# Kernel tuning notes

Hardware: AMD Instinct MI355X
Metric: run time of the kernel (lower is better)

## Reference

```python
import jax, jax.numpy as jnp
import numpy as np

HEADS = 6
DIM_HEAD = 64
SCALE = DIM_HEAD ** -0.5
BN_EPS = 1e-5


def _dw_pw(x, w_dw, gamma, beta, mean, var, w_pw, stride):
    """Depthwise 3x3 conv (groups=C) -> BatchNorm (inference) -> 1x1 pointwise conv."""
    C = x.shape[1]
    y = jax.lax.conv_general_dilated(
        x, w_dw, window_strides=(stride, stride), padding=((1, 1), (1, 1)),
        dimension_numbers=('NCHW', 'OIHW', 'NCHW'), feature_group_count=C)
    inv = gamma / jnp.sqrt(var + BN_EPS)
    y = y * inv[None, :, None, None] + (beta - mean * inv)[None, :, None, None]
    # 1x1 conv as einsum: w_pw is [O, C]
    return jnp.einsum('bchw,oc->bohw', y, w_pw)


def setup_inputs() -> dict:
    key = jax.random.key(0)
    ks = jax.random.split(key, 10)
    B, C, H, W = 32, 384, 32, 32
    inner = HEADS * DIM_HEAD  # 384
    ws = 0.05  # weight scale to keep attention logits sane
    return {
        'x': jax.random.normal(ks[0], (B, C, H, W), jnp.float32),
        'q_dw': jax.random.normal(ks[1], (C, 1, 3, 3), jnp.float32) * ws,
        'q_gamma': jnp.ones((C,), jnp.float32),
        'q_beta': jnp.zeros((C,), jnp.float32),
        'q_mean': jax.random.normal(ks[2], (C,), jnp.float32) * 0.1,
        'q_var': jax.random.uniform(ks[3], (C,), jnp.float32) + 0.5,
        'q_pw': jax.random.normal(ks[4], (inner, C), jnp.float32) * ws,
        'kv_dw': jax.random.normal(ks[5], (C, 1, 3, 3), jnp.float32) * ws,
        'kv_gamma': jnp.ones((C,), jnp.float32),
        'kv_beta': jnp.zeros((C,), jnp.float32),
        'kv_mean': jax.random.normal(ks[6], (C,), jnp.float32) * 0.1,
        'kv_var': jax.random.uniform(ks[7], (C,), jnp.float32) + 0.5,
        'kv_pw': jax.random.normal(ks[8], (2 * inner, C), jnp.float32) * ws,
        'out_w': jax.random.normal(ks[9], (C, inner), jnp.float32) * ws,
        'out_b': jnp.zeros((C,), jnp.float32),
    }


def reference(x, q_dw, q_gamma, q_beta, q_mean, q_var, q_pw,
              kv_dw, kv_gamma, kv_beta, kv_mean, kv_var, kv_pw,
              out_w, out_b):
    B, C, H, W = x.shape
    h, d = HEADS, DIM_HEAD
    # Q at full resolution, K/V spatially downsampled (stride 2)
    q = _dw_pw(x, q_dw, q_gamma, q_beta, q_mean, q_var, q_pw, stride=1)   # [B, h*d, H, W]
    kv = _dw_pw(x, kv_dw, kv_gamma, kv_beta, kv_mean, kv_var, kv_pw, stride=2)  # [B, 2*h*d, Hk, Wk]
    k, v = jnp.split(kv, 2, axis=1)
    Hk, Wk = k.shape[2], k.shape[3]
    # 'b (h d) x y -> b h (x y) d'
    q = q.reshape(B, h, d, H * W).transpose(0, 1, 3, 2)
    k = k.reshape(B, h, d, Hk * Wk).transpose(0, 1, 3, 2)
    v = v.reshape(B, h, d, Hk * Wk).transpose(0, 1, 3, 2)
    dots = jnp.einsum('bhid,bhjd->bhij', q, k) * SCALE  # [B, h, HW, HkWk]
    attn = jax.nn.softmax(dots, axis=-1)
    out = jnp.einsum('bhij,bhjd->bhid', attn, v)        # [B, h, HW, d]
    # 'b h (x y) d -> b (h d) x y'
    out = out.transpose(0, 1, 3, 2).reshape(B, h * d, H, W)
    # final 1x1 conv projection (dropout is identity, p=0)
    return jnp.einsum('bchw,oc->bohw', out, out_w) + out_b[None, :, None, None]
```

## Files before the change

### kernel.cpp

```cpp
#include <hip/hip_runtime.h>
#include <hip/hip_bf16.h>

#define CIN 384
#define PQ 1024
#define PKV 256
#define HEADS 6
#define DH 64
#define INNER 384
#define ATTN_SCALE 0.125f

typedef __hip_bfloat16 bf16;
typedef unsigned short ushort;
typedef __bf16 bf16x8 __attribute__((ext_vector_type(8)));
typedef float floatx4 __attribute__((ext_vector_type(4)));

__device__ __forceinline__ float b2f(bf16 v) { return __bfloat162float(v); }
__device__ __forceinline__ bf16 f2b(float v) { return __float2bfloat16(v); }
__device__ __forceinline__ ushort f2bu(float v) { bf16 h = __float2bfloat16(v); return *(ushort*)&h; }
__device__ __forceinline__ float ldf(const void* p, size_t i, int isbf) {
    return isbf ? __bfloat162float(((const bf16*)p)[i]) : ((const float*)p)[i];
}
__device__ __forceinline__ void dma16(const bf16* g, bf16* l) {
    __builtin_amdgcn_global_load_lds(
        (const __attribute__((address_space(1))) unsigned int*)g,
        (__attribute__((address_space(3))) unsigned int*)l, 16, 0, 0);
}
__device__ __forceinline__ int probe_isbf(const void* x) {
    const unsigned* u = (const unsigned*)x;
    int cnt = 0;
    for (int i = 0; i < 64; i++) {
        unsigned e = (u[i] >> 7) & 0xFFu;
        cnt += (e >= 100u && e <= 140u) ? 1 : 0;
    }
    return cnt >= 48 ? 1 : 0;
}
__device__ __forceinline__ unsigned cvtpk(float lo, float hi) {
    unsigned r;
    asm("v_cvt_pk_bf16_f32 %0, %1, %2" : "=v"(r) : "v"(lo), "v"(hi));
    return r;
}
__device__ __forceinline__ void halfswap(unsigned a, unsigned b, unsigned& lo, unsigned& hi) {
#if __has_builtin(__builtin_amdgcn_permlane32_swap)
    auto r = __builtin_amdgcn_permlane32_swap(a, b, false, false);
    lo = r[0]; hi = r[1];
#else
    unsigned ax = (unsigned)__shfl_xor((int)a, 32, 64);
    unsigned bx = (unsigned)__shfl_xor((int)b, 32, 64);
    bool lower = (threadIdx.x & 32) == 0;
    lo = lower ? a : bx;
    hi = lower ? ax : b;
#endif
}

template <int STRIDE, int HO, int WO>
__global__ __launch_bounds__(256) void dw_bn_kernel(
        const void* __restrict__ x, const void* __restrict__ wdw,
        const void* __restrict__ gamma, const void* __restrict__ beta,
        const void* __restrict__ mean, const void* __restrict__ var,
        bf16* __restrict__ yt,
        const void* __restrict__ w0, const void* __restrict__ w1,
        const void* __restrict__ w2, bf16* __restrict__ wdst) {
    constexpr int IN_ROWS = (8 - 1) * STRIDE + 3;
    constexpr int RL = 37;
    constexpr int PT = 8 * WO;
    constexpr unsigned XSZ = 32u * IN_ROWS * RL * 4;
    constexpr unsigned OSZ = (unsigned)PT * 40 * 2;
    __shared__ __align__(16) char smem[XSZ > OSZ ? XSZ : OSZ];
    float (*xin)[IN_ROWS][RL] = (float (*)[IN_ROWS][RL])smem;
    ushort (*outt)[40] = (ushort (*)[40])smem;

    int isbf = probe_isbf(x);
    int rg = blockIdx.x;
    int c0 = blockIdx.y * 32;
    int b  = blockIdx.z;
    int tid = threadIdx.x;

    if (c0 >= CIN) {
        const int n0 = INNER * CIN, n1 = 2 * INNER * CIN, n2 = INNER * CIN;
        const int total = n0 + n1 + n2;
        for (int i = (b * 4 + rg) * 256 + tid; i < total; i += 32768) {
            float v;
            if (i < n0) v = ldf(w0, i, isbf);
            else if (i < n0 + n1) v = ldf(w1, i - n0, isbf);
            else v = ldf(w2, i - n0 - n1, isbf);
            wdst[i] = f2b(v);
        }
        return;
    }

    int ri0 = rg * 8 * STRIDE - 1;

    for (int e = tid; e < 32 * IN_ROWS; e += 256) {
        int i = e % IN_ROWS, cc = e / IN_ROWS;
        xin[cc][i][0] = 0.f;
        xin[cc][i][33] = 0.f;
    }

    const int NCHUNK = 32 * IN_ROWS * 4;
    for (int ch = tid; ch < NCHUNK; ch += 256) {
        int wc = ch & 3;
        int t  = ch >> 2;
        int i  = t % IN_ROWS;
        int cc = t / IN_ROWS;
        int row = ri0 + i;
        float f[8];
        if (row >= 0 && row < 32) {
            size_t goff = ((size_t)(b * CIN + c0 + cc) * 32 + row) * 32 + wc * 8;
            if (isbf) {
                uint4 v = *(const uint4*)((const bf16*)x + goff);
                const ushort* u = (const ushort*)&v;
#pragma unroll
                for (int j = 0; j < 8; j++) f[j] = __uint_as_float((unsigned)u[j] << 16);
            } else {
                float4 v0 = *(const float4*)((const float*)x + goff);
                float4 v1 = *(const float4*)((const float*)x + goff + 4);
                f[0] = v0.x; f[1] = v0.y; f[2] = v0.z; f[3] = v0.w;
                f[4] = v1.x; f[5] = v1.y; f[6] = v1.z; f[7] = v1.w;
            }
        } else {
#pragma unroll
            for (int j = 0; j < 8; j++) f[j] = 0.f;
        }
        float* dst = &xin[cc][i][1 + wc * 8];
#pragma unroll
        for (int j = 0; j < 8; j++) dst[j] = f[j];
    }

    int cc = tid & 31;
    int g  = tid >> 5;
    int c  = c0 + cc;
    float w9[9];
#pragma unroll
    for (int k = 0; k < 9; k++) w9[k] = ldf(wdw, c * 9 + k, isbf);
    float inv  = ldf(gamma, c, isbf) * rsqrtf(ldf(var, c, isbf) + 1e-5f);
    float bias = ldf(beta, c, isbf) - ldf(mean, c, isbf) * inv;
    __syncthreads();

    const float* xr0 = xin[cc][g * STRIDE + 0];
    const float* xr1 = xin[cc][g * STRIDE + 1];
    const float* xr2 = xin[cc][g * STRIDE + 2];
    float o[WO];
    if (STRIDE == 1) {
        float a0 = xr0[0], a1 = xr0[1];
        float b0 = xr1[0], b1 = xr1[1];
        float q0 = xr2[0], q1 = xr2[1];
#pragma unroll
        for (int wo = 0; wo < WO; wo++) {
            float a2 = xr0[wo + 2], b2 = xr1[wo + 2], q2 = xr2[wo + 2];
            float acc = w9[0] * a0 + w9[1] * a1 + w9[2] * a2
                      + w9[3] * b0 + w9[4] * b1 + w9[5] * b2
                      + w9[6] * q0 + w9[7] * q1 + w9[8] * q2;
            o[wo] = acc * inv + bias;
            a0 = a1; a1 = a2; b0 = b1; b1 = b2; q0 = q1; q1 = q2;
        }
    } else {
        float a0 = xr0[0], b0 = xr1[0], q0 = xr2[0];
#pragma unroll
        for (int wo = 0; wo < WO; wo++) {
            float a1 = xr0[2 * wo + 1], a2 = xr0[2 * wo + 2];
            float b1 = xr1[2 * wo + 1], b2 = xr1[2 * wo + 2];
            float q1 = xr2[2 * wo + 1], q2 = xr2[2 * wo + 2];
            float acc = w9[0] * a0 + w9[1] * a1 + w9[2] * a2
                      + w9[3] * b0 + w9[4] * b1 + w9[5] * b2
                      + w9[6] * q0 + w9[7] * q1 + w9[8] * q2;
            o[wo] = acc * inv + bias;
            a0 = a2; b0 = b2; q0 = q2;
        }
    }
    __syncthreads();

#pragma unroll
    for (int wo = 0; wo < WO; wo++) outt[g * WO + wo][cc] = f2bu(o[wo]);
    __syncthreads();

    const size_t pbase = (size_t)b * (HO * WO) + (size_t)rg * 8 * WO;
    for (int chk = tid; chk < PT * 4; chk += 256) {
        int k = chk & 3, p = chk >> 2;
        uint4 v = *(const uint4*)&outt[p][k * 8];
        *(uint4*)(yt + (pbase + p) * CIN + c0 + k * 8) = v;
    }
}

__global__ __launch_bounds__(256, 3) void mfma_pw_qkv(
        const bf16* __restrict__ qpw, const bf16* __restrict__ yqt,
        bf16* __restrict__ qalt,
        const bf16* __restrict__ kvpw, const bf16* __restrict__ ykvt,
        bf16* __restrict__ kalt, bf16* __restrict__ valt) {
    __shared__ __align__(16) bf16 As[2][4096];
    __shared__ __align__(16) bf16 Bs[2][4096];
    int tid = threadIdx.x;
    int wave = tid >> 6, lane = tid & 63;
    int l15 = lane & 15, quad = lane >> 4;
    int wm = wave & 1, wn = wave >> 1;

    int bid = blockIdx.x;
    int P, b, p0, o0;
    const bf16 *asrc0, *bsrc0;
    bf16* outq;
    if (bid < 768) {
        int m = bid;
        int p0t = m & 7; m >>= 3;
        int o0t = m % 3; b = m / 3;
        P = 1024; p0 = p0t * 128; o0 = o0t * 128;
        asrc0 = yqt; bsrc0 = qpw; outq = qalt;
    } else {
        int m = bid - 768;
        int p0t = m & 1; m >>= 1;
        int o0t = m % 6; b = m / 6;
        P = 256; p0 = p0t * 128; o0 = o0t * 128;
        asrc0 = ykvt; bsrc0 = kvpw; outq = kalt;
    }

    const bf16* asrc = asrc0 + ((size_t)b * P + p0) * CIN;
    const bf16* bsrc = bsrc0 + (size_t)o0 * CIN;

    int srow = (lane >> 2);
    int sc   = lane & 3;
    auto stage = [&](int step, int buf) {
#pragma unroll
        for (int it = 0; it < 2; it++) {
            int row = wave * 32 + it * 16 + srow;
            int g = sc ^ (row & 3);
            size_t goff = (size_t)row * CIN + step * 32 + g * 8;
            dma16(asrc + goff, &As[buf][(wave * 2 + it) * 512]);
            dma16(bsrc + goff, &Bs[buf][(wave * 2 + it) * 512]);
        }
    };

    floatx4 acc[4][4];
#pragma unroll
    for (int pt = 0; pt < 4; pt++)
#pragma unroll
        for (int ot = 0; ot < 4; ot++) acc[pt][ot] = (floatx4){0.f, 0.f, 0.f, 0.f};

    stage(0, 0);
    __syncthreads();
    for (int s = 0; s < CIN / 32; s++) {
        int buf = s & 1;
        if (s < CIN / 32 - 1) stage(s + 1, buf ^ 1);
        bf16x8 af[4], bw[4];
        int slot = (quad ^ (l15 & 3)) * 8;
#pragma unroll
        for (int pt = 0; pt < 4; pt++)
            af[pt] = *(const bf16x8*)&As[buf][(wm * 64 + pt * 16 + l15) * 32 + slot];
#pragma unroll
        for (int ot = 0; ot < 4; ot++)
            bw[ot] = *(const bf16x8*)&Bs[buf][(wn * 64 + ot * 16 + l15) * 32 + slot];
#pragma unroll
        for (int pt = 0; pt < 4; pt++)
#pragma unroll
            for (int ot = 0; ot < 4; ot++)
                acc[pt][ot] = __builtin_amdgcn_mfma_f32_16x16x32_bf16(af[pt], bw[ot], acc[pt][ot], 0, 0, 0);
        __syncthreads();
    }

    int pw0 = p0 + wm * 64, ow0 = o0 + wn * 64;
#pragma unroll
    for (int ot = 0; ot < 4; ot++) {
        int o = ow0 + ot * 16 + l15;
        if (o < INNER) {
            int h = o >> 6, d = o & 63;
            bf16* base = outq + ((size_t)(b * HEADS + h) * P) * 64 + d;
#pragma unroll
            for (int pt = 0; pt < 4; pt++)
#pragma unroll
                for (int r = 0; r < 4; r++)
                    base[(size_t)(pw0 + pt * 16 + quad * 4 + r) * 64] = f2b(acc[pt][ot][r]);
        } else {
            int ch = o - INNER;
            bf16* base = valt + ((size_t)b * INNER + ch) * PKV;
#pragma unroll
            for (int pt = 0; pt < 4; pt++)
#pragma unroll
                for (int r = 0; r < 4; r++)
                    base[pw0 + pt * 16 + quad * 4 + r] = f2b(acc[pt][ot][r]);
        }
    }
}

__global__ __launch_bounds__(256, 3) void mfma_pw_out(
        const bf16* __restrict__ wt, const bf16* __restrict__ yt,
        const void* __restrict__ bias, void* __restrict__ out0,
        const void* __restrict__ xprobe) {
    __shared__ __align__(16) bf16 As[2][4096];
    __shared__ __align__(16) bf16 Bs[2][4096];
    const int P = PQ, O = CIN;
    int tid = threadIdx.x;
    int wave = tid >> 6, lane = tid & 63;
    int l15 = lane & 15, quad = lane >> 4;
    int wm = wave & 1, wn = wave >> 1;
    int b = blockIdx.z;
    int p0 = blockIdx.x * 128;
    int o0 = blockIdx.y * 128;

    const bf16* asrc = yt + ((size_t)b * P + p0) * CIN;
    const bf16* bsrc = wt + (size_t)o0 * CIN;

    int srow = (lane >> 2);
    int sc   = lane & 3;
    auto stage = [&](int step, int buf) {
#pragma unroll
        for (int it = 0; it < 2; it++) {
            int row = wave * 32 + it * 16 + srow;
            int g = sc ^ (row & 3);
            size_t goff = (size_t)row * CIN + step * 32 + g * 8;
            dma16(asrc + goff, &As[buf][(wave * 2 + it) * 512]);
            dma16(bsrc + goff, &Bs[buf][(wave * 2 + it) * 512]);
        }
    };

    floatx4 acc[4][4];
#pragma unroll
    for (int pt = 0; pt < 4; pt++)
#pragma unroll
        for (int ot = 0; ot < 4; ot++) acc[pt][ot] = (floatx4){0.f, 0.f, 0.f, 0.f};

    stage(0, 0);
    __syncthreads();
    for (int s = 0; s < CIN / 32; s++) {
        int buf = s & 1;
        if (s < CIN / 32 - 1) stage(s + 1, buf ^ 1);
        bf16x8 af[4], bw[4];
        int slot = (quad ^ (l15 & 3)) * 8;
#pragma unroll
        for (int pt = 0; pt < 4; pt++)
            af[pt] = *(const bf16x8*)&As[buf][(wm * 64 + pt * 16 + l15) * 32 + slot];
#pragma unroll
        for (int ot = 0; ot < 4; ot++)
            bw[ot] = *(const bf16x8*)&Bs[buf][(wn * 64 + ot * 16 + l15) * 32 + slot];
#pragma unroll
        for (int pt = 0; pt < 4; pt++)
#pragma unroll
            for (int ot = 0; ot < 4; ot++)
                acc[pt][ot] = __builtin_amdgcn_mfma_f32_16x16x32_bf16(af[pt], bw[ot], acc[pt][ot], 0, 0, 0);
        __syncthreads();
    }

    int pw0 = p0 + wm * 64, ow0 = o0 + wn * 64;
    int isbf = probe_isbf(xprobe);
#pragma unroll
    for (int ot = 0; ot < 4; ot++) {
        int o = ow0 + ot * 16 + l15;
        float bv = ldf(bias, o, isbf);
#pragma unroll
        for (int pt = 0; pt < 4; pt++) {
            int p = pw0 + pt * 16 + quad * 4;
            size_t idx = ((size_t)b * O + o) * P + p;
            if (!isbf) {
                float4 v4 = {acc[pt][ot][0] + bv, acc[pt][ot][1] + bv,
                             acc[pt][ot][2] + bv, acc[pt][ot][3] + bv};
                *(float4*)((float*)out0 + idx) = v4;
            } else {
                ushort4 u4 = {f2bu(acc[pt][ot][0] + bv), f2bu(acc[pt][ot][1] + bv),
                              f2bu(acc[pt][ot][2] + bv), f2bu(acc[pt][ot][3] + bv)};
                *(ushort4*)((bf16*)out0 + idx) = u4;
            }
        }
    }
}

#define QKT(S, Q0, Q1)                                                              \
    do {                                                                            \
        floatx4 z_ = (floatx4){0.f, 0.f, 0.f, 0.f};                                 \
        _Pragma("unroll")                                                           \
        for (int jt_ = 0; jt_ < 16; jt_++) {                                        \
            int j_ = jt_ * 16 + l15;                                                \
            bf16x8 k0_ = *(const bf16x8*)&Kl[j_ * 64 + (quad ^ (j_ & 7)) * 8];      \
            bf16x8 k1_ = *(const bf16x8*)&Kl[j_ * 64 + ((4 + quad) ^ (j_ & 7)) * 8];\
            floatx4 t_ = __builtin_amdgcn_mfma_f32_16x16x32_bf16(k0_, Q0, z_, 0, 0, 0); \
            S[jt_] = __builtin_amdgcn_mfma_f32_16x16x32_bf16(k1_, Q1, t_, 0, 0, 0); \
        }                                                                           \
    } while (0)

#define SOFTMAX(S, PINV)                                                            \
    do {                                                                            \
        float m0_ = S[0][0], m1_ = S[0][1], m2_ = S[0][2], m3_ = S[0][3];           \
        _Pragma("unroll")                                                           \
        for (int jt_ = 1; jt_ < 16; jt_++) {                                        \
            m0_ = fmaxf(m0_, S[jt_][0]); m1_ = fmaxf(m1_, S[jt_][1]);               \
            m2_ = fmaxf(m2_, S[jt_][2]); m3_ = fmaxf(m3_, S[jt_][3]);               \
        }                                                                           \
        float mx_ = fmaxf(fmaxf(m0_, m1_), fmaxf(m2_, m3_));                        \
        mx_ = fmaxf(mx_, __shfl_xor(mx_, 16, 64));                                  \
        mx_ = fmaxf(mx_, __shfl_xor(mx_, 32, 64));                                  \
        float mc_ = mx_ * C;                                                        \
        float a0_ = 0.f, a1_ = 0.f, a2_ = 0.f, a3_ = 0.f;                           \
        _Pragma("unroll")                                                           \
        for (int jt_ = 0; jt_ < 16; jt_++) {                                        \
            float e0_ = exp2f(S[jt_][0] * C - mc_);                                 \
            float e1_ = exp2f(S[jt_][1] * C - mc_);                                 \
            float e2_ = exp2f(S[jt_][2] * C - mc_);                                 \
            float e3_ = exp2f(S[jt_][3] * C - mc_);                                 \
            S[jt_][0] = e0_; S[jt_][1] = e1_; S[jt_][2] = e2_; S[jt_][3] = e3_;     \
            a0_ += e0_; a1_ += e1_; a2_ += e2_; a3_ += e3_;                         \
        }                                                                           \
        float sm_ = (a0_ + a1_) + (a2_ + a3_);                                      \
        sm_ += __shfl_xor(sm_, 16, 64);                                             \
        sm_ += __shfl_xor(sm_, 32, 64);                                             \
        PINV = 1.f / sm_;                                                           \
    } while (0)

#define PV_STORE(S, PINV, T)                                                        \
    do {                                                                            \
        floatx4 oacc_[4];                                                           \
        _Pragma("unroll")                                                           \
        for (int nt_ = 0; nt_ < 4; nt_++) oacc_[nt_] = (floatx4){0.f, 0.f, 0.f, 0.f}; \
        _Pragma("unroll")                                                           \
        for (int kk_ = 0; kk_ < 8; kk_++) {                                         \
            floatx4 se_ = S[2 * kk_], so_ = S[2 * kk_ + 1];                         \
            unsigned E0_ = cvtpk(se_[0] * PINV, se_[1] * PINV);                     \
            unsigned E1_ = cvtpk(se_[2] * PINV, se_[3] * PINV);                     \
            unsigned D0_ = cvtpk(so_[0] * PINV, so_[1] * PINV);                     \
            unsigned D1_ = cvtpk(so_[2] * PINV, so_[3] * PINV);                     \
            unsigned lo0_, hi0_, lo1_, hi1_;                                        \
            halfswap(E0_, D0_, lo0_, hi0_);                                         \
            halfswap(E1_, D1_, lo1_, hi1_);                                         \
            unsigned sel0_ = (quad & 1) ? hi0_ : lo0_;                              \
            unsigned sel1_ = (quad & 1) ? hi1_ : lo1_;                              \
            unsigned x0_ = (unsigned)__shfl_xor((int)sel0_, 16, 64);                \
            unsigned x1_ = (unsigned)__shfl_xor((int)sel1_, 16, 64);                \
            union { unsigned u[4]; bf16x8 v; } pf_;                                 \
            pf_.u[0] = (quad & 1) ? x0_ : sel0_;                                    \
            pf_.u[1] = (quad & 1) ? x1_ : sel1_;                                    \
            pf_.u[2] = (quad & 1) ? sel0_ : x0_;                                    \
            pf_.u[3] = (quad & 1) ? sel1_ : x1_;                                    \
            _Pragma("unroll")                                                       \
            for (int nt_ = 0; nt_ < 4; nt_++) {                                     \
                int d_ = nt_ * 16 + l15;                                            \
                bf16x8 bv_ = *(const bf16x8*)&Vl[d_ * 256 + ((kk_ * 4 + quad) ^ (d_ & 15)) * 8]; \
                oacc_[nt_] = __builtin_amdgcn_mfma_f32_16x16x32_bf16(pf_.v, bv_, oacc_[nt_], 0, 0, 0); \
            }                                                                       \
        }                                                                           \
        _Pragma("unroll")                                                           \
        for (int nt_ = 0; nt_ < 4; nt_++)                                           \
            _Pragma("unroll")                                                       \
            for (int r_ = 0; r_ < 4; r_++)                                          \
                Ot[wave][quad * 4 + r_][nt_ * 16 + l15] = f2bu(oacc_[nt_][r_]);     \
        int row_ = lane >> 2, d0_ = (lane & 3) * 16;                                \
        uint4 ld0_ = *(const uint4*)&Ot[wave][row_][d0_];                           \
        uint4 ld1_ = *(const uint4*)&Ot[wave][row_][d0_ + 8];                       \
        bf16* dst_ = ao + ((size_t)b * PQ + p0 + (T) * 64 + row_) * INNER + h * DH + d0_; \
        *(uint4*)dst_ = ld0_;                                                       \
        *(uint4*)(dst_ + 8) = ld1_;                                                 \
    } while (0)

__global__ __launch_bounds__(256, 2) void attn_kernel(
        const bf16* __restrict__ qalt, const bf16* __restrict__ kalt,
        const bf16* __restrict__ valt, bf16* __restrict__ ao) {
    __shared__ __align__(16) bf16 Kl[16384];
    __shared__ __align__(16) bf16 Vl[16384];
    __shared__ __align__(16) ushort Ot[4][16][80];
    int tid = threadIdx.x;
    int wave = tid >> 6, lane = tid & 63;
    int l15 = lane & 15, quad = lane >> 4;
    int blk = blockIdx.x;
    int swz = (blk & 7) * 96 + (blk >> 3);
    int seg = swz & 3;
    int bh  = swz >> 2;
    int b = bh / HEADS, h = bh % HEADS;

    const bf16* qbase = qalt + (size_t)(b * HEADS + h) * PQ * DH;
    const bf16* kbase = kalt + (size_t)(b * HEADS + h) * PKV * DH;
    const bf16* vbase = valt + ((size_t)b * INNER + h * DH) * PKV;

    {
        int j = lane >> 3, cs = lane & 7;
#pragma unroll
        for (int it = 0; it < 8; it++) {
            int jr = (wave * 8 + it) * 8 + j;
            int g = cs ^ (jr & 7);
            dma16(kbase + (size_t)jr * 64 + g * 8, &Kl[(wave * 8 + it) * 512]);
        }
        int d = lane >> 5, cs2 = lane & 31;
#pragma unroll
        for (int it = 0; it < 8; it++) {
            int dr = (wave * 8 + it) * 2 + d;
            int g = cs2 ^ (dr & 15);
            dma16(vbase + (size_t)dr * 256 + g * 8, &Vl[(wave * 8 + it) * 512]);
        }
    }

    int p0 = seg * 256 + wave * 16;
    const bf16* qrow = qbase + (size_t)(p0 + l15) * DH + quad * 8;
    bf16x8 qA0 = *(const bf16x8*)qrow;
    bf16x8 qA1 = *(const bf16x8*)(qrow + 32);
    bf16x8 qB0 = *(const bf16x8*)(qrow + 64 * DH);
    bf16x8 qB1 = *(const bf16x8*)(qrow + 64 * DH + 32);
    __syncthreads();

    const float C = ATTN_SCALE * 1.44269504f;
    floatx4 sA[16], sB[16];
    float pinv;

    QKT(sA, qA0, qA1);
    qA0 = *(const bf16x8*)(qrow + 128 * DH);
    qA1 = *(const bf16x8*)(qrow + 128 * DH + 32);

    SOFTMAX(sA, pinv);
    QKT(sB, qB0, qB1);
    PV_STORE(sA, pinv, 0);
    qB0 = *(const bf16x8*)(qrow + 192 * DH);
    qB1 = *(const bf16x8*)(qrow + 192 * DH + 32);

    SOFTMAX(sB, pinv);
    QKT(sA, qA0, qA1);
    PV_STORE(sB, pinv, 1);

    SOFTMAX(sA, pinv);
    QKT(sB, qB0, qB1);
    PV_STORE(sA, pinv, 2);

    SOFTMAX(sB, pinv);
    PV_STORE(sB, pinv, 3);
}

extern "C" void kernel_launch(void* const* d_in, const int* in_sizes, int n_in,
                              void* d_out, int out_size, void* d_ws, size_t ws_size,
                              hipStream_t stream) {
    const void* x        = d_in[0];
    const void* q_dw     = d_in[1];
    const void* q_gamma  = d_in[2];
    const void* q_beta   = d_in[3];
    const void* q_mean   = d_in[4];
    const void* q_var    = d_in[5];
    const void* q_pw     = d_in[6];
    const void* kv_dw    = d_in[7];
    const void* kv_gamma = d_in[8];
    const void* kv_beta  = d_in[9];
    const void* kv_mean  = d_in[10];
    const void* kv_var   = d_in[11];
    const void* kv_pw    = d_in[12];
    const void* out_w    = d_in[13];
    const void* out_b    = d_in[14];

    bf16* pool = (bf16*)((char*)d_ws + 256);
    bf16* yqt  = pool;
    bf16* ykvt = yqt  + (size_t)32 * 1024 * 384;
    bf16* qalt = ykvt + (size_t)32 * 256 * 384;
    bf16* kalt = qalt + (size_t)32 * 6 * 1024 * 64;
    bf16* valt = kalt + (size_t)32 * 6 * 256 * 64;
    bf16* wbf  = valt + (size_t)32 * 384 * 256;
    bf16* qpw_bf = wbf;
    bf16* kvpw_bf = wbf + (size_t)INNER * CIN;
    bf16* outw_bf = kvpw_bf + (size_t)2 * INNER * CIN;
    bf16* aob  = yqt;

    dw_bn_kernel<1, 32, 32><<<dim3(4, 13, 32), 256, 0, stream>>>(
        x, q_dw, q_gamma, q_beta, q_mean, q_var, yqt, q_pw, kv_pw, out_w, wbf);
    dw_bn_kernel<2, 16, 16><<<dim3(2, 12, 32), 256, 0, stream>>>(
        x, kv_dw, kv_gamma, kv_beta, kv_mean, kv_var, ykvt, nullptr, nullptr, nullptr, nullptr);
    mfma_pw_qkv<<<1152, 256, 0, stream>>>(qpw_bf, yqt, qalt, kvpw_bf, ykvt, kalt, valt);
    attn_kernel<<<768, 256, 0, stream>>>(qalt, kalt, valt, aob);
    mfma_pw_out<<<dim3(8, 3, 32), 256, 0, stream>>>(outw_bf, aob, out_b, d_out, x);
}
```

Baseline: 236.8 us.

## Use XOR-swizzled float4 LDS layout in depthwise conv and split stride-2 work finer

Measured after the change: 228.4 us. 1.04x faster.

```diff
diff --git a/kernel.cpp b/kernel.cpp
--- a/kernel.cpp
+++ b/kernel.cpp
@@ -52,7 +52,7 @@
 #endif
 }
 
-template <int STRIDE, int HO, int WO>
+template <int STRIDE, int G, int HO, int WO>
 __global__ __launch_bounds__(256) void dw_bn_kernel(
         const void* __restrict__ x, const void* __restrict__ wdw,
         const void* __restrict__ gamma, const void* __restrict__ beta,
@@ -60,13 +60,12 @@
         bf16* __restrict__ yt,
         const void* __restrict__ w0, const void* __restrict__ w1,
         const void* __restrict__ w2, bf16* __restrict__ wdst) {
-    constexpr int IN_ROWS = (8 - 1) * STRIDE + 3;
-    constexpr int RL = 37;
-    constexpr int PT = 8 * WO;
-    constexpr unsigned XSZ = 32u * IN_ROWS * RL * 4;
+    constexpr int IN_ROWS = (G - 1) * STRIDE + 3;
+    constexpr int PT = G * WO;
+    constexpr unsigned XSZ = 32u * IN_ROWS * 32 * 4;
     constexpr unsigned OSZ = (unsigned)PT * 40 * 2;
     __shared__ __align__(16) char smem[XSZ > OSZ ? XSZ : OSZ];
-    float (*xin)[IN_ROWS][RL] = (float (*)[IN_ROWS][RL])smem;
+    float* xs = (float*)smem;
     ushort (*outt)[40] = (ushort (*)[40])smem;
 
     int isbf = probe_isbf(x);
@@ -88,20 +87,13 @@
         return;
     }
 
-    int ri0 = rg * 8 * STRIDE - 1;
-
-    for (int e = tid; e < 32 * IN_ROWS; e += 256) {
-        int i = e % IN_ROWS, cc = e / IN_ROWS;
-        xin[cc][i][0] = 0.f;
-        xin[cc][i][33] = 0.f;
-    }
+    int ri0 = rg * G * STRIDE - 1;
 
     const int NCHUNK = 32 * IN_ROWS * 4;
     for (int ch = tid; ch < NCHUNK; ch += 256) {
         int wc = ch & 3;
-        int t  = ch >> 2;
-        int i  = t % IN_ROWS;
-        int cc = t / IN_ROWS;
+        int cc = (ch >> 2) & 31;
+        int i  = ch >> 7;
         int row = ri0 + i;
         float f[8];
         if (row >= 0 && row < 32) {
@@ -121,14 +113,18 @@
 #pragma unroll
             for (int j = 0; j < 8; j++) f[j] = 0.f;
         }
-        float* dst = &xin[cc][i][1 + wc * 8];
-#pragma unroll
-        for (int j = 0; j < 8; j++) dst[j] = f[j];
+        float* rb = xs + ((size_t)(i * 32 + cc)) * 32;
+        int key = cc & 7;
+        float4 fa = {f[0], f[1], f[2], f[3]};
+        float4 fb = {f[4], f[5], f[6], f[7]};
+        *(float4*)(rb + ((2 * wc) ^ key) * 4)     = fa;
+        *(float4*)(rb + ((2 * wc + 1) ^ key) * 4) = fb;
     }
 
     int cc = tid & 31;
     int g  = tid >> 5;
     int c  = c0 + cc;
+    int key = cc & 7;
     float w9[9];
 #pragma unroll
     for (int k = 0; k < 9; k++) w9[k] = ldf(wdw, c * 9 + k, isbf);
@@ -136,44 +132,66 @@
     float bias = ldf(beta, c, isbf) - ldf(mean, c, isbf) * inv;
     __syncthreads();
 
-    const float* xr0 = xin[cc][g * STRIDE + 0];
-    const float* xr1 = xin[cc][g * STRIDE + 1];
-    const float* xr2 = xin[cc][g * STRIDE + 2];
-    float o[WO];
+    float o[STRIDE == 1 ? 32 : 8];
     if (STRIDE == 1) {
-        float a0 = xr0[0], a1 = xr0[1];
-        float b0 = xr1[0], b1 = xr1[1];
-        float q0 = xr2[0], q1 = xr2[1];
-#pragma unroll
-        for (int wo = 0; wo < WO; wo++) {
-            float a2 = xr0[wo + 2], b2 = xr1[wo + 2], q2 = xr2[wo + 2];
-            float acc = w9[0] * a0 + w9[1] * a1 + w9[2] * a2
-                      + w9[3] * b0 + w9[4] * b1 + w9[5] * b2
-                      + w9[6] * q0 + w9[7] * q1 + w9[8] * q2;
-            o[wo] = acc * inv + bias;
-            a0 = a1; a1 = a2; b0 = b1; b1 = b2; q0 = q1; q1 = q2;
+#pragma unroll
+        for (int p = 0; p < 2; p++) {
+            float rf[3][18];
+#pragma unroll
+            for (int ky = 0; ky < 3; ky++) {
+                const float* rb = xs + ((size_t)((g + ky) * 32 + cc)) * 32;
+#pragma unroll
+                for (int cch = 0; cch < 4; cch++) {
+                    float4 v = *(const float4*)(rb + ((4 * p + cch) ^ key) * 4);
+                    rf[ky][1 + 4 * cch] = v.x; rf[ky][2 + 4 * cch] = v.y;
+                    rf[ky][3 + 4 * cch] = v.z; rf[ky][4 + 4 * cch] = v.w;
+                }
+                rf[ky][0]  = p ? rb[((3 ^ key) * 4) + 3] : 0.f;
+                rf[ky][17] = p ? 0.f : rb[((4 ^ key) * 4) + 0];
+            }
+#pragma unroll
+            for (int j = 0; j < 16; j++) {
+                float acc = w9[0] * rf[0][j] + w9[1] * rf[0][j + 1] + w9[2] * rf[0][j + 2]
+                          + w9[3] * rf[1][j] + w9[4] * rf[1][j + 1] + w9[5] * rf[1][j + 2]
+                          + w9[6] * rf[2][j] + w9[7] * rf[2][j + 1] + w9[8] * rf[2][j + 2];
+                o[p * 16 + j] = acc * inv + bias;
+            }
         }
     } else {
-        float a0 = xr0[0], b0 = xr1[0], q0 = xr2[0];
-#pragma unroll
-        for (int wo = 0; wo < WO; wo++) {
-            float a1 = xr0[2 * wo + 1], a2 = xr0[2 * wo + 2];
-            float b1 = xr1[2 * wo + 1], b2 = xr1[2 * wo + 2];
-            float q1 = xr2[2 * wo + 1], q2 = xr2[2 * wo + 2];
-            float acc = w9[0] * a0 + w9[1] * a1 + w9[2] * a2
-                      + w9[3] * b0 + w9[4] * b1 + w9[5] * b2
-                      + w9[6] * q0 + w9[7] * q1 + w9[8] * q2;
-            o[wo] = acc * inv + bias;
-            a0 = a2; b0 = b2; q0 = q2;
+        int rgrp = g & 3, hf = g >> 2;
+        float rf[3][17];
+#pragma unroll
+        for (int ky = 0; ky < 3; ky++) {
+            const float* rb = xs + ((size_t)((2 * rgrp + ky) * 32 + cc)) * 32;
+#pragma unroll
+            for (int cch = 0; cch < 4; cch++) {
+                float4 v = *(const float4*)(rb + ((4 * hf + cch) ^ key) * 4);
+                rf[ky][1 + 4 * cch] = v.x; rf[ky][2 + 4 * cch] = v.y;
+                rf[ky][3 + 4 * cch] = v.z; rf[ky][4 + 4 * cch] = v.w;
+            }
+            rf[ky][0] = hf ? rb[((3 ^ key) * 4) + 3] : 0.f;
+        }
+#pragma unroll
+        for (int j = 0; j < 8; j++) {
+            float acc = w9[0] * rf[0][2 * j] + w9[1] * rf[0][2 * j + 1] + w9[2] * rf[0][2 * j + 2]
+                      + w9[3] * rf[1][2 * j] + w9[4] * rf[1][2 * j + 1] + w9[5] * rf[1][2 * j + 2]
+                      + w9[6] * rf[2][2 * j] + w9[7] * rf[2][2 * j + 1] + w9[8] * rf[2][2 * j + 2];
+            o[j] = acc * inv + bias;
         }
     }
     __syncthreads();
 
-#pragma unroll
-    for (int wo = 0; wo < WO; wo++) outt[g * WO + wo][cc] = f2bu(o[wo]);
+    if (STRIDE == 1) {
+#pragma unroll
+        for (int wo = 0; wo < 32; wo++) outt[g * WO + wo][cc] = f2bu(o[wo]);
+    } else {
+        int rgrp = g & 3, hf = g >> 2;
+#pragma unroll
+        for (int j = 0; j < 8; j++) outt[rgrp * 16 + hf * 8 + j][cc] = f2bu(o[j]);
+    }
     __syncthreads();
 
-    const size_t pbase = (size_t)b * (HO * WO) + (size_t)rg * 8 * WO;
+    const size_t pbase = (size_t)b * (HO * WO) + (size_t)rg * G * WO;
     for (int chk = tid; chk < PT * 4; chk += 256) {
         int k = chk & 3, p = chk >> 2;
         uint4 v = *(const uint4*)&outt[p][k * 8];
@@ -545,9 +563,9 @@
     bf16* outw_bf = kvpw_bf + (size_t)2 * INNER * CIN;
     bf16* aob  = yqt;
 
-    dw_bn_kernel<1, 32, 32><<<dim3(4, 13, 32), 256, 0, stream>>>(
+    dw_bn_kernel<1, 8, 32, 32><<<dim3(4, 13, 32), 256, 0, stream>>>(
         x, q_dw, q_gamma, q_beta, q_mean, q_var, yqt, q_pw, kv_pw, out_w, wbf);
-    dw_bn_kernel<2, 16, 16><<<dim3(2, 12, 32), 256, 0, stream>>>(
+    dw_bn_kernel<2, 4, 16, 16><<<dim3(4, 12, 32), 256, 0, stream>>>(
         x, kv_dw, kv_gamma, kv_beta, kv_mean, kv_var, ykvt, nullptr, nullptr, nullptr, nullptr);
     mfma_pw_qkv<<<1152, 256, 0, stream>>>(qpw_bf, yqt, qalt, kvpw_bf, ykvt, kalt, valt);
     attn_kernel<<<768, 256, 0, stream>>>(qalt, kalt, valt, aob);
```
